# Optimization experiments

Measured on AMD Instinct MI355X. Metric: run time of the kernel, lower is better.

Reference implementation:

```python
import jax, jax.numpy as jnp
import numpy as np

N_EMBDS = 1024
N_HEADS = 16
HEAD_DIM = N_EMBDS // N_HEADS


def setup_inputs() -> dict:
    key = jax.random.key(0)
    ks = jax.random.split(key, 5)
    B, T, C = 2, 2048, N_EMBDS
    x = jax.random.normal(ks[0], (B, T, C), dtype=jnp.float32)
    s = 1.0 / np.sqrt(C)
    W_attn = jax.random.normal(ks[1], (C, 3 * C), dtype=jnp.float32) * s
    b_attn = jnp.zeros((3 * C,), dtype=jnp.float32)
    W_proj = jax.random.normal(ks[2], (C, C), dtype=jnp.float32) * s
    b_proj = jnp.zeros((C,), dtype=jnp.float32)
    return {"x": x, "W_attn": W_attn, "b_attn": b_attn, "W_proj": W_proj, "b_proj": b_proj}


def reference(x, W_attn, b_attn, W_proj, b_proj):
    B, T, C = x.shape
    H, D = N_HEADS, HEAD_DIM
    qkv = x @ W_attn + b_attn  # [B, T, 3C]
    q, k, v = jnp.split(qkv, 3, axis=-1)
    # [B, H, T, D]
    q = q.reshape(B, T, H, D).transpose(0, 2, 1, 3)
    k = k.reshape(B, T, H, D).transpose(0, 2, 1, 3)
    v = v.reshape(B, T, H, D).transpose(0, 2, 1, 3)
    att = jnp.einsum('bhqd,bhkd->bhqk', q, k) * (1.0 / np.sqrt(D))  # [B,H,T,T]
    causal = jnp.tril(jnp.ones((T, T), dtype=bool))
    att = jnp.where(causal[None, None], att, -jnp.inf)
    att = jax.nn.softmax(att, axis=-1)
    y = jnp.einsum('bhqk,bhkd->bhqd', att, v)  # [B,H,T,D]
    y = y.transpose(0, 2, 1, 3).reshape(B, T, C)
    return y @ W_proj + b_proj
```

## Files before the change

kernel.cpp:

```cpp
#include <hip/hip_runtime.h>
#include <hip/hip_bf16.h>


typedef __bf16 bf16x8 __attribute__((ext_vector_type(8)));
typedef float  f32x4  __attribute__((ext_vector_type(4)));
#define BF16 __hip_bfloat16

constexpr int Bb = 2, Tt = 2048, Cc = 1024, Hh = 16, Dd = 64;
constexpr float NEG_INF = -1e30f;
constexpr float Q_SCALE = 0.18033688011112042f;
constexpr float EXP2_BIAS = 17.312340490667562f;

__device__ __forceinline__ f32x4 mfma16(bf16x8 a, bf16x8 b, f32x4 c) {
  return __builtin_amdgcn_mfma_f32_16x16x32_bf16(a, b, c, 0, 0, 0);
}

__device__ __forceinline__ float fast_exp2(float x) {
  float r;
  asm("v_exp_f32 %0, %1" : "=v"(r) : "v"(x));
  return r;
}

__device__ __forceinline__ void gll16(const void* g, void* l) {
  __builtin_amdgcn_global_load_lds((const __attribute__((address_space(1))) void*)g,
                                   (__attribute__((address_space(3))) void*)l,
                                   16, 0, 0);
}

__device__ __forceinline__ int swz64(int r, int c) {
  return r * 64 + ((((c >> 3) ^ r) & 7) << 3) + (c & 7);
}

__device__ __forceinline__ int kperm_inv(int r) {
  return (r & 0x23) | ((r & 0x0C) << 1) | ((r & 0x10) >> 2);
}

__global__ void prep_kernel(const float* __restrict__ x, BF16* __restrict__ xb,
                            const float* __restrict__ Wa, BF16* __restrict__ WaT,
                            const float* __restrict__ Wp, BF16* __restrict__ WpT) {
  __shared__ float tile[32][33];
  const int bx = blockIdx.x, tid = threadIdx.x;
  if (bx < 2048) {
    const int i = (bx * 256 + tid) * 8;
    const float4 a = *(const float4*)&x[i];
    const float4 b = *(const float4*)&x[i + 4];
    BF16 o[8];
    o[0] = __float2bfloat16(a.x); o[1] = __float2bfloat16(a.y);
    o[2] = __float2bfloat16(a.z); o[3] = __float2bfloat16(a.w);
    o[4] = __float2bfloat16(b.x); o[5] = __float2bfloat16(b.y);
    o[6] = __float2bfloat16(b.z); o[7] = __float2bfloat16(b.w);
    *(uint4*)&xb[i] = *(const uint4*)o;
    return;
  }
  const float* in; BF16* outT; int K, N, gx, gy;
  if (bx < 5120) {
    const int idx = bx - 2048;
    in = Wa; outT = WaT; K = 1024; N = 3072; gx = idx % 96; gy = idx / 96;
  } else {
    const int idx = bx - 5120;
    in = Wp; outT = WpT; K = 1024; N = 1024; gx = idx % 32; gy = idx / 32;
  }
  const int n0 = gx * 32, k0 = gy * 32;
  const int tx = tid & 31, ty = tid >> 5;
#pragma unroll
  for (int i = ty; i < 32; i += 8) tile[i][tx] = in[(size_t)(k0 + i) * N + (n0 + tx)];
  __syncthreads();
#pragma unroll
  for (int i = ty; i < 32; i += 8)
    outT[(size_t)(n0 + i) * K + (k0 + tx)] = __float2bfloat16(tile[tx][i]);
}

template <int MODE>
__global__ __launch_bounds__(256) void gemm_bt(const BF16* __restrict__ A,
                                               const BF16* __restrict__ Bt,
                                               const float* __restrict__ bias,
                                               BF16* __restrict__ oq,
                                               BF16* __restrict__ ok,
                                               BF16* __restrict__ ov,
                                               float* __restrict__ fout,
                                               int Ndim, int Kdim) {
  __shared__ alignas(16) BF16 sA[128 * 64];
  __shared__ alignas(16) BF16 sB[128 * 64];
  const int tid = threadIdx.x;
  const int wave = tid >> 6, lane = tid & 63;
  const int quad = lane >> 4, l16 = lane & 15;
  const int wm = (wave >> 1) * 64, wn = (wave & 1) * 64;
  const int bm = blockIdx.y * 128, bn = blockIdx.x * 128;
  const int sw = l16 & 7;

  f32x4 acc[4][4];
#pragma unroll
  for (int i = 0; i < 4; ++i)
#pragma unroll
    for (int j = 0; j < 4; ++j) acc[i][j] = f32x4{0.f, 0.f, 0.f, 0.f};

  const int srow = wave * 32 + (lane >> 3);
  const int sgl = (lane ^ (lane >> 3)) & 7;
  const BF16* gA0 = &A[(size_t)(bm + srow) * Kdim + sgl * 8];
  const BF16* gB0 = &Bt[(size_t)(bn + srow) * Kdim + sgl * 8];
  const size_t rstep8 = (size_t)8 * Kdim;

  for (int k0 = 0; k0 < Kdim; k0 += 64) {
    __syncthreads();
#pragma unroll
    for (int s = 0; s < 4; ++s) {
      gll16(gA0 + s * rstep8 + k0, &sA[wave * 2048 + s * 512]);
      gll16(gB0 + s * rstep8 + k0, &sB[wave * 2048 + s * 512]);
    }
    __syncthreads();

#pragma unroll
    for (int h = 0; h < 2; ++h) {
      bf16x8 af[4], bf_[4];
#pragma unroll
      for (int i = 0; i < 4; ++i)
        af[i] = *(const bf16x8*)
            &sA[(wm + i * 16 + l16) * 64 + (((h * 4 + quad) ^ sw) << 3)];
#pragma unroll
      for (int j = 0; j < 4; ++j)
        bf_[j] = *(const bf16x8*)
            &sB[(wn + j * 16 + l16) * 64 + (((h * 4 + quad) ^ sw) << 3)];
#pragma unroll
      for (int i = 0; i < 4; ++i)
#pragma unroll
        for (int j = 0; j < 4; ++j) acc[i][j] = mfma16(af[i], bf_[j], acc[i][j]);
    }
  }

#pragma unroll
  for (int j = 0; j < 4; ++j) {
    const int gn = bn + wn + j * 16 + l16;
    const float bsv = bias[gn];
    if (MODE == 1) {
#pragma unroll
      for (int i = 0; i < 4; ++i)
#pragma unroll
        for (int r = 0; r < 4; ++r) {
          const int gm = bm + wm + i * 16 + quad * 4 + r;
          fout[(size_t)gm * Ndim + gn] = acc[i][j][r] + bsv;
        }
    } else {
      const int which = (bn + wn + j * 16) >> 10;
      const int c = gn & 1023;
      const int hh = c >> 6, dd = c & 63;
#pragma unroll
      for (int i = 0; i < 4; ++i) {
        const int gm0 = bm + wm + i * 16 + quad * 4;
        const int bb = gm0 >> 11, tk0 = gm0 & 2047;
        const size_t bh = (size_t)(bb * Hh + hh);
        if (which == 2) {
          BF16 tmp[4];
#pragma unroll
          for (int r = 0; r < 4; ++r) tmp[r] = __float2bfloat16(acc[i][j][r] + bsv);
          *(uint2*)&ov[(bh * Dd + dd) * Tt + tk0] = *(const uint2*)tmp;
        } else {
          BF16* dst = (which == 0) ? oq : ok;
          const float scale = (which == 0) ? Q_SCALE : 1.0f;
#pragma unroll
          for (int r = 0; r < 4; ++r)
            dst[(bh * Tt + tk0 + r) * Dd + dd] =
                __float2bfloat16((acc[i][j][r] + bsv) * scale);
        }
      }
    }
  }
}

__global__ __launch_bounds__(256) void attn_kernel(const BF16* __restrict__ qg,
                                                   const BF16* __restrict__ kg,
                                                   const BF16* __restrict__ vtg,
                                                   BF16* __restrict__ yb) {
  __shared__ alignas(16) BF16 sK[2 * 64 * 64];
  __shared__ alignas(16) BF16 sV[2 * 64 * 64];
  const int id = blockIdx.x;
  const int xcd = id & 7, local = id >> 3;
  const int bh = xcd * 4 + (local & 3);
  const int s = 31 - (local >> 2);
  const int b = bh >> 4, h = bh & 15;
  const int tid = threadIdx.x;
  const int wave = tid >> 6, lane = tid & 63;
  const int quad = lane >> 4, l16 = lane & 15;
  const size_t base = ((size_t)(b * Hh + h)) * Tt * Dd;
  const int qrow0 = s * 64 + wave * 16;

  bf16x8 qf0, qf1;
  {
    const size_t off = base + (size_t)(qrow0 + l16) * Dd;
    qf0 = *(const bf16x8*)&qg[off + quad * 8];
    qf1 = *(const bf16x8*)&qg[off + 32 + quad * 8];
  }

  bf16x8 ones8;
#pragma unroll
  for (int j = 0; j < 8; ++j) ones8[j] = (__bf16)1.0f;

  f32x4 o[4], oL;
#pragma unroll
  for (int i = 0; i < 4; ++i) o[i] = f32x4{0.f, 0.f, 0.f, 0.f};
  oL = f32x4{0.f, 0.f, 0.f, 0.f};

  const f32x4 cbias = f32x4{-EXP2_BIAS, -EXP2_BIAS, -EXP2_BIAS, -EXP2_BIAS};

  const int lr = lane >> 3;
  const int swg = (lane ^ (lane >> 3)) & 7;
  const int r0 = wave * 16 + lr, r1 = r0 + 8;
  const BF16* pk0 = &kg[base + (size_t)kperm_inv(r0) * Dd + swg * 8];
  const BF16* pk1 = &kg[base + (size_t)kperm_inv(r1) * Dd + swg * 8];
  const BF16* pv0 = &vtg[base + (size_t)r0 * Tt + swg * 8];
  const BF16* pv1 = &vtg[base + (size_t)r1 * Tt + swg * 8];
  const int dst0 = wave * 1024, dst1 = dst0 + 512;

  gll16(pk0, &sK[dst0]);
  gll16(pk1, &sK[dst1]);
  gll16(pv0, &sV[dst0]);
  gll16(pv1, &sV[dst1]);

  for (int jt = 0; jt <= s; ++jt) {
    asm volatile("s_waitcnt vmcnt(0)" ::: "memory");
    __builtin_amdgcn_s_barrier();
    const BF16* sKb = &sK[(jt & 1) * 4096];
    const BF16* sVb = &sV[(jt & 1) * 4096];
    if (jt < s) {
      const int nb = ((jt + 1) & 1) * 4096;
      const size_t ko = (size_t)(jt + 1) * 4096;
      const int vo = (jt + 1) * 64;
      gll16(pk0 + ko, &sK[nb + dst0]);
      gll16(pk1 + ko, &sK[nb + dst1]);
      gll16(pv0 + vo, &sV[nb + dst0]);
      gll16(pv1 + vo, &sV[nb + dst1]);
    }
    const int kb = jt * 64;

    f32x4 sS[4];
    __builtin_amdgcn_s_setprio(1);
#pragma unroll
    for (int t = 0; t < 4; ++t) {
      const bf16x8 kf0 = *(const bf16x8*)&sKb[swz64(t * 16 + l16, quad * 8)];
      const bf16x8 kf1 = *(const bf16x8*)&sKb[swz64(t * 16 + l16, 32 + quad * 8)];
      sS[t] = mfma16(kf0, qf0, cbias);
      sS[t] = mfma16(kf1, qf1, sS[t]);
    }
    __builtin_amdgcn_s_setprio(0);

    if (jt == s) {
      const int q = qrow0 + l16;
#pragma unroll
      for (int t = 0; t < 4; ++t) {
        const int kc0 = kb + (t >> 1) * 32 + quad * 8 + (t & 1) * 4;
#pragma unroll
        for (int r = 0; r < 4; ++r)
          if (kc0 + r > q) sS[t][r] = NEG_INF;
      }
    }

    bf16x8 pf[2];
#pragma unroll
    for (int cc = 0; cc < 2; ++cc)
#pragma unroll
      for (int j = 0; j < 8; ++j)
        pf[cc][j] = (__bf16)fast_exp2(sS[cc * 2 + (j >> 2)][j & 3]);

    __builtin_amdgcn_s_setprio(1);
#pragma unroll
    for (int cc = 0; cc < 2; ++cc) {
#pragma unroll
      for (int dt = 0; dt < 4; ++dt) {
        const bf16x8 vb =
            *(const bf16x8*)&sVb[swz64(dt * 16 + l16, cc * 32 + quad * 8)];
        o[dt] = mfma16(pf[cc], vb, o[dt]);
      }
      oL = mfma16(pf[cc], ones8, oL);
    }
    __builtin_amdgcn_s_setprio(0);
  }

#pragma unroll
  for (int r = 0; r < 4; ++r) {
    const float inv = 1.0f / oL[r];
    const int trow = qrow0 + quad * 4 + r;
#pragma unroll
    for (int dt = 0; dt < 4; ++dt)
      yb[((size_t)(b * Tt + trow)) * Cc + h * Dd + dt * 16 + l16] =
          __float2bfloat16(o[dt][r] * inv);
  }
}

extern "C" void kernel_launch(void* const* d_in, const int* in_sizes, int n_in,
                              void* d_out, int out_size, void* d_ws, size_t ws_size,
                              hipStream_t stream) {
  (void)in_sizes; (void)n_in; (void)out_size; (void)ws_size;
  const float* x      = (const float*)d_in[0];
  const float* W_attn = (const float*)d_in[1];
  const float* b_attn = (const float*)d_in[2];
  const float* W_proj = (const float*)d_in[3];
  const float* b_proj = (const float*)d_in[4];
  float* out = (float*)d_out;

  constexpr size_t SZ_WA = (size_t)3072 * 1024;
  constexpr size_t SZ_WP = (size_t)1024 * 1024;
  constexpr size_t SZ_X  = (size_t)4096 * 1024;
  constexpr size_t SZ_T  = (size_t)Bb * Hh * Tt * Dd;

  BF16* ws   = (BF16*)d_ws;
  BF16* wtAb = ws;
  BF16* wtPb = wtAb + SZ_WA;
  BF16* xb   = wtPb + SZ_WP;
  BF16* q    = xb + SZ_X;
  BF16* k    = q + SZ_T;
  BF16* vt   = k + SZ_T;
  BF16* yb   = vt + SZ_T;

  prep_kernel<<<dim3(6144), 256, 0, stream>>>(x, xb, W_attn, wtAb, W_proj, wtPb);
  gemm_bt<0><<<dim3(24, 32), 256, 0, stream>>>(xb, wtAb, b_attn, q, k, vt, nullptr,
                                               3072, 1024);
  attn_kernel<<<dim3(1024), 256, 0, stream>>>(q, k, vt, yb);
  gemm_bt<1><<<dim3(8, 32), 256, 0, stream>>>(yb, wtPb, b_proj, nullptr, nullptr,
                                              nullptr, out, 1024, 1024);
}
```

Before: 173.4 us.

## Process 128-key tiles per iteration in causal attention loop

```diff
diff --git a/kernel.cpp b/kernel.cpp
--- a/kernel.cpp
+++ b/kernel.cpp
@@ -27,12 +27,8 @@
                                    16, 0, 0);
 }
 
-__device__ __forceinline__ int swz64(int r, int c) {
-  return r * 64 + ((((c >> 3) ^ r) & 7) << 3) + (c & 7);
-}
-
-__device__ __forceinline__ int kperm_inv(int r) {
-  return (r & 0x23) | ((r & 0x0C) << 1) | ((r & 0x10) >> 2);
+__device__ __forceinline__ int kperm_inv7(int r) {
+  return (r & 0x63) | ((r & 0x0C) << 1) | ((r & 0x10) >> 2);
 }
 
 __global__ void prep_kernel(const float* __restrict__ x, BF16* __restrict__ xb,
@@ -170,8 +166,8 @@
                                                    const BF16* __restrict__ kg,
                                                    const BF16* __restrict__ vtg,
                                                    BF16* __restrict__ yb) {
-  __shared__ alignas(16) BF16 sK[2 * 64 * 64];
-  __shared__ alignas(16) BF16 sV[2 * 64 * 64];
+  __shared__ alignas(16) BF16 sK[2 * 8192];
+  __shared__ alignas(16) BF16 sV[2 * 8192];
   const int id = blockIdx.x;
   const int xcd = id & 7, local = id >> 3;
   const int bh = xcd * 4 + (local & 3);
@@ -182,6 +178,7 @@
   const int quad = lane >> 4, l16 = lane & 15;
   const size_t base = ((size_t)(b * Hh + h)) * Tt * Dd;
   const int qrow0 = s * 64 + wave * 16;
+  const int sw = l16 & 7;
 
   bf16x8 qf0, qf1;
   {
@@ -201,78 +198,83 @@
 
   const f32x4 cbias = f32x4{-EXP2_BIAS, -EXP2_BIAS, -EXP2_BIAS, -EXP2_BIAS};
 
-  const int lr = lane >> 3;
-  const int swg = (lane ^ (lane >> 3)) & 7;
-  const int r0 = wave * 16 + lr, r1 = r0 + 8;
-  const BF16* pk0 = &kg[base + (size_t)kperm_inv(r0) * Dd + swg * 8];
-  const BF16* pk1 = &kg[base + (size_t)kperm_inv(r1) * Dd + swg * 8];
-  const BF16* pv0 = &vtg[base + (size_t)r0 * Tt + swg * 8];
-  const BF16* pv1 = &vtg[base + (size_t)r1 * Tt + swg * 8];
-  const int dst0 = wave * 1024, dst1 = dst0 + 512;
-
-  gll16(pk0, &sK[dst0]);
-  gll16(pk1, &sK[dst1]);
-  gll16(pv0, &sV[dst0]);
-  gll16(pv1, &sV[dst1]);
-
-  for (int jt = 0; jt <= s; ++jt) {
+  const int t = tid;
+  const int sgk = (t ^ (t >> 3)) & 7;
+  const int sgv = (t ^ (t >> 4)) & 15;
+  const BF16* pk[4];
+  const BF16* pv[4];
+#pragma unroll
+  for (int i = 0; i < 4; ++i) {
+    pk[i] = &kg[base + (size_t)kperm_inv7(i * 32 + (t >> 3)) * Dd + sgk * 8];
+    pv[i] = &vtg[base + (size_t)(i * 16 + (t >> 4)) * Tt + sgv * 8];
+  }
+
+#define STAGE(buf, jt_)                                            \
+  do {                                                             \
+    const size_t ko_ = (size_t)(jt_) * (128 * Dd);                 \
+    const int vo_ = (jt_) * 128;                                   \
+    _Pragma("unroll") for (int i_ = 0; i_ < 4; ++i_) {             \
+      gll16(pk[i_] + ko_, &sK[(buf) * 8192 + i_ * 2048 + t * 8]);  \
+      gll16(pv[i_] + vo_, &sV[(buf) * 8192 + i_ * 2048 + t * 8]);  \
+    }                                                              \
+  } while (0)
+
+  const int nt = (s + 2) >> 1;
+  STAGE(0, 0);
+
+  for (int jt = 0; jt < nt; ++jt) {
     asm volatile("s_waitcnt vmcnt(0)" ::: "memory");
     __builtin_amdgcn_s_barrier();
-    const BF16* sKb = &sK[(jt & 1) * 4096];
-    const BF16* sVb = &sV[(jt & 1) * 4096];
-    if (jt < s) {
-      const int nb = ((jt + 1) & 1) * 4096;
-      const size_t ko = (size_t)(jt + 1) * 4096;
-      const int vo = (jt + 1) * 64;
-      gll16(pk0 + ko, &sK[nb + dst0]);
-      gll16(pk1 + ko, &sK[nb + dst1]);
-      gll16(pv0 + vo, &sV[nb + dst0]);
-      gll16(pv1 + vo, &sV[nb + dst1]);
-    }
-    const int kb = jt * 64;
-
-    f32x4 sS[4];
+    const BF16* sKb = &sK[(jt & 1) * 8192];
+    const BF16* sVb = &sV[(jt & 1) * 8192];
+    if (jt < nt - 1) STAGE((jt + 1) & 1, jt + 1);
+
+    f32x4 sS[8];
     __builtin_amdgcn_s_setprio(1);
 #pragma unroll
-    for (int t = 0; t < 4; ++t) {
-      const bf16x8 kf0 = *(const bf16x8*)&sKb[swz64(t * 16 + l16, quad * 8)];
-      const bf16x8 kf1 = *(const bf16x8*)&sKb[swz64(t * 16 + l16, 32 + quad * 8)];
-      sS[t] = mfma16(kf0, qf0, cbias);
-      sS[t] = mfma16(kf1, qf1, sS[t]);
+    for (int tt = 0; tt < 8; ++tt) {
+      const bf16x8 kf0 =
+          *(const bf16x8*)&sKb[(tt * 16 + l16) * 64 + ((quad ^ sw) << 3)];
+      const bf16x8 kf1 =
+          *(const bf16x8*)&sKb[(tt * 16 + l16) * 64 + (((4 + quad) ^ sw) << 3)];
+      sS[tt] = mfma16(kf0, qf0, cbias);
+      sS[tt] = mfma16(kf1, qf1, sS[tt]);
     }
     __builtin_amdgcn_s_setprio(0);
 
-    if (jt == s) {
+    if (jt == nt - 1) {
       const int q = qrow0 + l16;
-#pragma unroll
-      for (int t = 0; t < 4; ++t) {
-        const int kc0 = kb + (t >> 1) * 32 + quad * 8 + (t & 1) * 4;
+      const int kb = jt * 128;
+#pragma unroll
+      for (int tt = 0; tt < 8; ++tt) {
+        const int kc0 = kb + (tt >> 1) * 32 + quad * 8 + (tt & 1) * 4;
 #pragma unroll
         for (int r = 0; r < 4; ++r)
-          if (kc0 + r > q) sS[t][r] = NEG_INF;
+          if (kc0 + r > q) sS[tt][r] = NEG_INF;
       }
     }
 
-    bf16x8 pf[2];
-#pragma unroll
-    for (int cc = 0; cc < 2; ++cc)
+    bf16x8 pf[4];
+#pragma unroll
+    for (int cc = 0; cc < 4; ++cc)
 #pragma unroll
       for (int j = 0; j < 8; ++j)
         pf[cc][j] = (__bf16)fast_exp2(sS[cc * 2 + (j >> 2)][j & 3]);
 
     __builtin_amdgcn_s_setprio(1);
 #pragma unroll
-    for (int cc = 0; cc < 2; ++cc) {
+    for (int cc = 0; cc < 4; ++cc) {
 #pragma unroll
       for (int dt = 0; dt < 4; ++dt) {
-        const bf16x8 vb =
-            *(const bf16x8*)&sVb[swz64(dt * 16 + l16, cc * 32 + quad * 8)];
+        const bf16x8 vb = *(const bf16x8*)
+            &sVb[(dt * 16 + l16) * 128 + ((((cc * 4 + quad) ^ l16) & 15) << 3)];
         o[dt] = mfma16(pf[cc], vb, o[dt]);
       }
       oL = mfma16(pf[cc], ones8, oL);
     }
     __builtin_amdgcn_s_setprio(0);
   }
+#undef STAGE
 
 #pragma unroll
   for (int r = 0; r < 4; ++r) {
```

New measurement: 173.1 us. No clear change (-0.2%).
